# Kernel tuning notes

Measured on AMD Instinct MI355X. Metric: run time of the kernel, lower is better.

The kernel has to match this reference:

```python
import jax, jax.numpy as jnp
import numpy as np

EPS = 1e-12  # F.normalize default eps


def _l2_normalize(x, axis):
    n = jnp.sqrt(jnp.sum(x * x, axis=axis, keepdims=True))
    return x / jnp.maximum(n, EPS)


def setup_inputs() -> dict:
    key = jax.random.key(0)
    ks = jax.random.split(key, 13)
    b, n, d, h = 8, 4096, 1024, 16
    scale = 0.02
    inp = {
        "query": jax.random.normal(ks[0], (b, n, d), jnp.float32),
        "key": jax.random.normal(ks[1], (b, n, d), jnp.float32),
        "value": jax.random.normal(ks[2], (b, n, d), jnp.float32),
        "key_padding_mask": jax.random.randint(ks[3], (b, n), 0, 2).astype(bool),
        "Wq": jax.random.normal(ks[4], (d, d), jnp.float32) * scale,
        "bq": jax.random.normal(ks[5], (d,), jnp.float32) * scale,
        "Wk": jax.random.normal(ks[6], (d, d), jnp.float32) * scale,
        "bk": jax.random.normal(ks[7], (d,), jnp.float32) * scale,
        "Wv": jax.random.normal(ks[8], (d, d), jnp.float32) * scale,
        "bv": jax.random.normal(ks[9], (d,), jnp.float32) * scale,
        "Wo": jax.random.normal(ks[10], (d, d), jnp.float32) * scale,
        "bo": jax.random.normal(ks[11], (d,), jnp.float32) * scale,
    }
    return inp


def reference(query, key, value, key_padding_mask, Wq, bq, Wk, bk, Wv, bv, Wo, bo):
    b, n, d = query.shape
    h = 16
    dh = d // h
    # projections (torch Linear: x @ W.T + b)
    q = query @ Wq.T + bq
    k = key @ Wk.T + bk
    v = value @ Wv.T + bv
    # elu feature map
    q = 1.0 + jax.nn.elu(q)
    k = 1.0 + jax.nn.elu(k)
    # zero out padded keys
    k = jnp.where(key_padding_mask[:, :, None], 0.0, k)
    # split heads: b n (h d) -> b h n d
    q = q.reshape(b, n, h, dh).transpose(0, 2, 1, 3)
    k = k.reshape(b, n, h, dh).transpose(0, 2, 1, 3)
    v = v.reshape(b, n, h, dh).transpose(0, 2, 1, 3)
    # faithful to source: q normalized over sequence axis, k over feature axis
    q = _l2_normalize(q, axis=2)
    k = _l2_normalize(k, axis=3)
    kv = jnp.einsum('bhnd,bhne->bhde', k, v)      # (b,h,dh,dh)
    out = jnp.einsum('bhnd,bhde->bhne', q, kv)    # (b,h,n,dh)
    out = out.transpose(0, 2, 1, 3).reshape(b, n, d)
    return out @ Wo.T + bo
```

## Files before the change

### kernel.cpp

```cpp
#include <hip/hip_runtime.h>


typedef unsigned short u16;
typedef __attribute__((ext_vector_type(8))) short short8;
typedef __attribute__((ext_vector_type(4))) float f32x4;

#define GAS __attribute__((address_space(1)))
#define LAS __attribute__((address_space(3)))

__device__ __forceinline__ u16 f2bf(float x) {
  unsigned u = __float_as_uint(x);
  u += 0x7fffu + ((u >> 16) & 1u);
  return (u16)(u >> 16);
}
__device__ __forceinline__ unsigned pack2(float a, float b) {
  return (unsigned)f2bf(a) | ((unsigned)f2bf(b) << 16);
}
__device__ __forceinline__ float bflo(unsigned w) { return __uint_as_float(w << 16); }
__device__ __forceinline__ float bfhi(unsigned w) { return __uint_as_float(w & 0xffff0000u); }

__global__ __launch_bounds__(256) void detect_mask(const unsigned* __restrict__ m,
                                                   int* __restrict__ flags) {
  int i = blockIdx.x * 256 + threadIdx.x;
  unsigned w = m[i];
  if (w & 0xFEFEFEFEu) atomicOr(&flags[1], 1);
  if (w & 0xFFFFFF00u) atomicOr(&flags[0], 1);
}

__global__ __launch_bounds__(256) void mask_cvt(const void* __restrict__ m,
                                                const int* __restrict__ flags,
                                                float* __restrict__ keep) {
  int i = blockIdx.x * 256 + threadIdx.x;
  bool pad;
  if (flags[1])      pad = ((const float*)m)[i] != 0.f;
  else if (flags[0]) pad = ((const unsigned char*)m)[i] != 0;
  else               pad = ((const int*)m)[i] != 0;
  keep[i] = pad ? 0.f : 1.f;
}

__device__ __forceinline__ void cvt_body(const float* __restrict__ src,
                                         u16* __restrict__ dst, int n4) {
  int i = blockIdx.x * blockDim.x + threadIdx.x;
  int stride = gridDim.x * blockDim.x;
  for (; i < n4; i += stride) {
    float4 v = ((const float4*)src)[i];
    ((uint2*)dst)[i] = make_uint2(pack2(v.x, v.y), pack2(v.z, v.w));
  }
}
__global__ __launch_bounds__(256) void cvt3(const float* __restrict__ s0, const float* __restrict__ s1,
                                            const float* __restrict__ s2,
                                            u16* __restrict__ d0, u16* __restrict__ d1,
                                            u16* __restrict__ d2, int n4) {
  const float* s = (blockIdx.z == 0) ? s0 : (blockIdx.z == 1) ? s1 : s2;
  u16* d = (blockIdx.z == 0) ? d0 : (blockIdx.z == 1) ? d1 : d2;
  cvt_body(s, d, n4);
}
__global__ __launch_bounds__(256) void cvt4(const float* __restrict__ s0, const float* __restrict__ s1,
                                            const float* __restrict__ s2, const float* __restrict__ s3,
                                            u16* __restrict__ d0, u16* __restrict__ d1,
                                            u16* __restrict__ d2, u16* __restrict__ d3, int n4) {
  const float* s = (blockIdx.z == 0) ? s0 : (blockIdx.z == 1) ? s1 : (blockIdx.z == 2) ? s2 : s3;
  u16* d = (blockIdx.z == 0) ? d0 : (blockIdx.z == 1) ? d1 : (blockIdx.z == 2) ? d2 : d3;
  cvt_body(s, d, n4);
}

template <int MODE>
__global__ __launch_bounds__(256) void gemm_bt(const u16* __restrict__ A,
                                               const u16* __restrict__ B0,
                                               const float* __restrict__ bias,
                                               void* __restrict__ Out,
                                               float* __restrict__ sacc,
                                               const float* __restrict__ keep) {
  constexpr int K = 1024;
  __shared__ __align__(16) u16 As[128 * 64];
  __shared__ __align__(16) u16 Bs[128 * 64];

  const int t = threadIdx.x;
  const int w = t >> 6, l = t & 63;
  const int wm = w & 1, wn = w >> 1;
  const int rowTile = blockIdx.y * 128;
  const int colTile = blockIdx.x * 128;
  const int bidx = blockIdx.y >> 5;

  const u16* B = (MODE == 3) ? (B0 + ((size_t)bidx << 20)) : B0;

  f32x4 acc[4][4] = {};

  const int lr = l >> 3;
  const int lc = (l & 7) << 3;
  const u16* aRow = A + (size_t)(rowTile + w * 32 + lr) * K + lc;
  const u16* bRow = B + (size_t)(colTile + w * 32 + lr) * K + lc;

  for (int kt = 0; kt < K / 64; ++kt) {
    const int k0 = kt * 64;
    __syncthreads();
#pragma unroll
    for (int s = 0; s < 4; ++s) {
      __builtin_amdgcn_global_load_lds((const GAS void*)(aRow + (size_t)s * 8 * K + k0),
                                       (LAS void*)&As[(w * 4 + s) * 512], 16, 0, 0);
      __builtin_amdgcn_global_load_lds((const GAS void*)(bRow + (size_t)s * 8 * K + k0),
                                       (LAS void*)&Bs[(w * 4 + s) * 512], 16, 0, 0);
    }
    __syncthreads();
#pragma unroll
    for (int kk = 0; kk < 2; ++kk) {
      short8 af[4], bf[4];
      const int ko = kk * 32 + ((l >> 4) << 3);
#pragma unroll
      for (int mb = 0; mb < 4; ++mb)
        af[mb] = *(const short8*)&As[(wm * 64 + mb * 16 + (l & 15)) * 64 + ko];
#pragma unroll
      for (int nb = 0; nb < 4; ++nb)
        bf[nb] = *(const short8*)&Bs[(wn * 64 + nb * 16 + (l & 15)) * 64 + ko];
#pragma unroll
      for (int mb = 0; mb < 4; ++mb)
#pragma unroll
        for (int nb = 0; nb < 4; ++nb)
          acc[mb][nb] = __builtin_amdgcn_mfma_f32_16x16x32_bf16(af[mb], bf[nb], acc[mb][nb], 0, 0, 0);
    }
  }

  const int qr = (l >> 4) << 2;
  const int cl = l & 15;
#pragma unroll
  for (int nb = 0; nb < 4; ++nb) {
    const int col = colTile + wn * 64 + nb * 16 + cl;
    const float bv = bias[col];
    float csum = 0.f;
#pragma unroll
    for (int mb = 0; mb < 4; ++mb) {
      const int rowb = rowTile + wm * 64 + mb * 16 + qr;
#pragma unroll
      for (int r = 0; r < 4; ++r) {
        float y = acc[mb][nb][r] + bv;
        if (MODE == 0 || MODE == 1) y = (y > 0.f) ? (y + 1.f) : __expf(y);
        if (MODE == 1) y *= keep[rowb + r];
        if (MODE == 3) ((float*)Out)[(size_t)(rowb + r) * 1024 + col] = y;
        else           ((u16*)Out)[(size_t)(rowb + r) * 1024 + col] = f2bf(y);
        if (MODE == 0) csum += y * y;
      }
    }
    if (MODE == 0) {
      csum += __shfl_xor(csum, 16);
      csum += __shfl_xor(csum, 32);
      if (l < 16) atomicAdd(&sacc[bidx * 1024 + colTile + wn * 64 + nb * 16 + l], csum);
    }
  }
}

__global__ __launch_bounds__(256, 2) void kv2(const u16* __restrict__ fk,
                                              const u16* __restrict__ fv,
                                              float* __restrict__ kvpart) {
  const int ch = blockIdx.x, h = blockIdx.y, b = blockIdx.z;
  __shared__ __align__(16) u16 smem[2 * 256 * 64];
  u16* lk = smem;
  u16* lv = smem + 256 * 64;
  const int t = threadIdx.x;
  const int w = t >> 6, l = t & 63;
  const int d8 = (l & 7) * 8, e8 = (l >> 3) * 8;
  float acc[64] = {};

  for (int sub = 0; sub < 4; ++sub) {
    const int i0 = ch * 1024 + sub * 256;
    __syncthreads();
    {
      const size_t g = ((size_t)(b * 4096 + i0 + t)) * 1024 + h * 64;
      const uint4* kp = (const uint4*)&fk[g];
      float kf[64];
#pragma unroll
      for (int j = 0; j < 8; ++j) {
        uint4 kq = kp[j];
        kf[j * 8 + 0] = bflo(kq.x); kf[j * 8 + 1] = bfhi(kq.x);
        kf[j * 8 + 2] = bflo(kq.y); kf[j * 8 + 3] = bfhi(kq.y);
        kf[j * 8 + 4] = bflo(kq.z); kf[j * 8 + 5] = bfhi(kq.z);
        kf[j * 8 + 6] = bflo(kq.w); kf[j * 8 + 7] = bfhi(kq.w);
      }
      float ss = 0.f;
#pragma unroll
      for (int j = 0; j < 64; ++j) ss += kf[j] * kf[j];
      const float inv = 1.f / fmaxf(sqrtf(ss), 1e-12f);
#pragma unroll
      for (int j = 0; j < 8; ++j) {
        uint4 o;
        o.x = pack2(kf[j * 8 + 0] * inv, kf[j * 8 + 1] * inv);
        o.y = pack2(kf[j * 8 + 2] * inv, kf[j * 8 + 3] * inv);
        o.z = pack2(kf[j * 8 + 4] * inv, kf[j * 8 + 5] * inv);
        o.w = pack2(kf[j * 8 + 6] * inv, kf[j * 8 + 7] * inv);
        *(uint4*)&lk[t * 64 + j * 8] = o;
      }
      const uint4* vp = (const uint4*)&fv[g];
#pragma unroll
      for (int j = 0; j < 8; ++j) *(uint4*)&lv[t * 64 + j * 8] = vp[j];
    }
    __syncthreads();
#pragma unroll 2
    for (int ii = 0; ii < 64; ++ii) {
      const int i = w * 64 + ii;
      uint4 kw4 = *(const uint4*)&lk[i * 64 + d8];
      uint4 vw4 = *(const uint4*)&lv[i * 64 + e8];
      float ka[8], va[8];
      ka[0] = bflo(kw4.x); ka[1] = bfhi(kw4.x); ka[2] = bflo(kw4.y); ka[3] = bfhi(kw4.y);
      ka[4] = bflo(kw4.z); ka[5] = bfhi(kw4.z); ka[6] = bflo(kw4.w); ka[7] = bfhi(kw4.w);
      va[0] = bflo(vw4.x); va[1] = bfhi(vw4.x); va[2] = bflo(vw4.y); va[3] = bfhi(vw4.y);
      va[4] = bflo(vw4.z); va[5] = bfhi(vw4.z); va[6] = bflo(vw4.w); va[7] = bfhi(vw4.w);
#pragma unroll
      for (int a = 0; a < 8; ++a)
#pragma unroll
        for (int c = 0; c < 8; ++c)
          acc[a * 8 + c] += ka[a] * va[c];
    }
  }

  __syncthreads();
  float* scratch = (float*)smem;
  if (w > 0) {
#pragma unroll
    for (int c = 0; c < 64; c += 4)
      *(float4*)&scratch[((w - 1) * 64 + l) * 64 + c] = *(float4*)&acc[c];
  }
  __syncthreads();
  if (w == 0) {
#pragma unroll
    for (int p = 0; p < 3; ++p)
#pragma unroll
      for (int c = 0; c < 64; c += 4) {
        float4 s = *(const float4*)&scratch[(p * 64 + l) * 64 + c];
        acc[c + 0] += s.x; acc[c + 1] += s.y; acc[c + 2] += s.z; acc[c + 3] += s.w;
      }
    float* dst = kvpart + (size_t)(((ch * 8 + b) * 16 + h)) * 4096;
#pragma unroll
    for (int a = 0; a < 8; ++a)
#pragma unroll
      for (int c = 0; c < 8; c += 4)
        *(float4*)&dst[(d8 + a) * 64 + e8 + c] = *(float4*)&acc[a * 8 + c];
  }
}

__global__ __launch_bounds__(256) void kv_reduce(const float* __restrict__ kvpart,
                                                 const float* __restrict__ sacc,
                                                 float* __restrict__ kvred) {
  const int bh = blockIdx.x;
  const int b = bh >> 4, h = bh & 15;
  const int t = threadIdx.x;
  const int d = t >> 2;
  const float invq = 1.f / fmaxf(sqrtf(sacc[b * 1024 + h * 64 + d]), 1e-12f);
#pragma unroll
  for (int j = 0; j < 4; ++j) {
    const size_t off = (size_t)bh * 4096 + t * 16 + j * 4;
    float4 s = *(const float4*)&kvpart[off];
#pragma unroll
    for (int ch = 1; ch < 4; ++ch) {
      float4 p = *(const float4*)&kvpart[(size_t)ch * 524288 + off];
      s.x += p.x; s.y += p.y; s.z += p.z; s.w += p.w;
    }
    s.x *= invq; s.y *= invq; s.z *= invq; s.w *= invq;
    *(float4*)&kvred[(size_t)bh * 4096 + t * 16 + j * 4] = s;
  }
}

__global__ __launch_bounds__(256) void scale_mt(const float* __restrict__ kvred,
                                                const u16* __restrict__ wob,
                                                u16* __restrict__ Mt) {
  const int jt = blockIdx.x, h = blockIdx.y, b = blockIdx.z;
  __shared__ float kvl[64 * 64];
  const int t = threadIdx.x;

  {
    const int d = t >> 2, cp = (t & 3) * 16;
    const float* src = kvred + (size_t)((b * 16 + h) * 4096) + d * 64 + cp;
#pragma unroll
    for (int c = 0; c < 16; c += 4)
      *(float4*)&kvl[d * 64 + cp + c] = *(const float4*)&src[c];
  }
  __syncthreads();

  const int j = jt * 128 + (t & 127);
  const int g = t >> 7;
  float wo[64];
  const u16* wp = wob + (size_t)j * 1024 + h * 64;
#pragma unroll
  for (int e8 = 0; e8 < 64; e8 += 8) {
    uint4 q = *(const uint4*)&wp[e8];
    wo[e8 + 0] = bflo(q.x); wo[e8 + 1] = bfhi(q.x);
    wo[e8 + 2] = bflo(q.y); wo[e8 + 3] = bfhi(q.y);
    wo[e8 + 4] = bflo(q.z); wo[e8 + 5] = bfhi(q.z);
    wo[e8 + 6] = bflo(q.w); wo[e8 + 7] = bfhi(q.w);
  }
  u16* op = Mt + ((size_t)b << 20) + (size_t)j * 1024 + h * 64 + g * 32;
#pragma unroll 4
  for (int dd = 0; dd < 32; ++dd) {
    const int drow = g * 32 + dd;
    float s = 0.f;
#pragma unroll
    for (int e = 0; e < 64; ++e) s += kvl[drow * 64 + e] * wo[e];
    op[dd] = f2bf(s);
  }
}

extern "C" void kernel_launch(void* const* d_in, const int* in_sizes, int n_in,
                              void* d_out, int out_size, void* d_ws, size_t ws_size,
                              hipStream_t stream) {
  const float* query = (const float*)d_in[0];
  const float* key   = (const float*)d_in[1];
  const float* value = (const float*)d_in[2];
  const void*  mask  = d_in[3];
  const float* Wq = (const float*)d_in[4];
  const float* bq = (const float*)d_in[5];
  const float* Wk = (const float*)d_in[6];
  const float* bk = (const float*)d_in[7];
  const float* Wv = (const float*)d_in[8];
  const float* bv = (const float*)d_in[9];
  const float* Wo = (const float*)d_in[10];
  const float* bo = (const float*)d_in[11];

  char* W = (char*)d_ws;
  int*   flags = (int*)W;
  float* sacc  = (float*)(W + 256);
  float* keep  = (float*)(W + 33024);
  u16* wqb = (u16*)(W + 164096);
  u16* wkb = wqb + 1048576;
  u16* wvb = wkb + 1048576;
  u16* wob = wvb + 1048576;
  u16* qb  = wob + 1048576;
  u16* kb  = qb + 33554432;
  u16* vb  = kb + 33554432;
  u16* fq  = vb + 33554432;
  u16* fk  = fq + 33554432;
  u16* fv  = fk + 33554432;
  u16* Mt = qb;
  float* kvpart = (float*)kb;
  float* kvred  = (float*)(kb + 4194304);

  hipMemsetAsync(d_ws, 0, 33024, stream);

  detect_mask<<<32, 256, 0, stream>>>((const unsigned*)mask, flags);
  mask_cvt<<<128, 256, 0, stream>>>(mask, flags, keep);

  cvt3<<<dim3(1024, 1, 3), 256, 0, stream>>>(query, key, value, qb, kb, vb, 8388608);
  cvt4<<<dim3(128, 1, 4), 256, 0, stream>>>(Wq, Wk, Wv, Wo, wqb, wkb, wvb, wob, 262144);

  dim3 gg(8, 256);
  gemm_bt<0><<<gg, 256, 0, stream>>>(qb, wqb, bq, fq, sacc, nullptr);
  gemm_bt<1><<<gg, 256, 0, stream>>>(kb, wkb, bk, fk, nullptr, keep);
  gemm_bt<2><<<gg, 256, 0, stream>>>(vb, wvb, bv, fv, nullptr, nullptr);

  kv2<<<dim3(4, 16, 8), 256, 0, stream>>>(fk, fv, kvpart);
  kv_reduce<<<128, 256, 0, stream>>>(kvpart, sacc, kvred);
  scale_mt<<<dim3(8, 16, 8), 256, 0, stream>>>(kvred, wob, Mt);

  gemm_bt<3><<<gg, 256, 0, stream>>>(fq, Mt, bo, d_out, nullptr, nullptr);
}
```

Before: 1.061 ms.

## Fuse fp32-to-bf16 input conversion into projection GEMM loads and remap tiles per XCD

Removes the separate cvt3 pass over query/key/value. The projection GEMMs now read fp32 activations directly, pack them to bf16 in registers and store them to LDS, which saves a full read-write round trip of three large tensors. The block index is also remapped so that each XCD handles a contiguous group of row tiles, aiming for better L2 reuse. In exchange, A-tile loads now go through registers instead of async global-to-LDS, and each A load moves twice the bytes without double buffering, which may expose more latency.

Result: faster. 991.4 us (-6.6%).

```diff
diff --git a/kernel.cpp b/kernel.cpp
--- a/kernel.cpp
+++ b/kernel.cpp
@@ -47,14 +47,6 @@
     ((uint2*)dst)[i] = make_uint2(pack2(v.x, v.y), pack2(v.z, v.w));
   }
 }
-__global__ __launch_bounds__(256) void cvt3(const float* __restrict__ s0, const float* __restrict__ s1,
-                                            const float* __restrict__ s2,
-                                            u16* __restrict__ d0, u16* __restrict__ d1,
-                                            u16* __restrict__ d2, int n4) {
-  const float* s = (blockIdx.z == 0) ? s0 : (blockIdx.z == 1) ? s1 : s2;
-  u16* d = (blockIdx.z == 0) ? d0 : (blockIdx.z == 1) ? d1 : d2;
-  cvt_body(s, d, n4);
-}
 __global__ __launch_bounds__(256) void cvt4(const float* __restrict__ s0, const float* __restrict__ s1,
                                             const float* __restrict__ s2, const float* __restrict__ s3,
                                             u16* __restrict__ d0, u16* __restrict__ d1,
@@ -65,7 +57,7 @@
 }
 
 template <int MODE>
-__global__ __launch_bounds__(256) void gemm_bt(const u16* __restrict__ A,
+__global__ __launch_bounds__(256) void gemm_bt(const void* __restrict__ Ain,
                                                const u16* __restrict__ B0,
                                                const float* __restrict__ bias,
                                                void* __restrict__ Out,
@@ -78,28 +70,57 @@
   const int t = threadIdx.x;
   const int w = t >> 6, l = t & 63;
   const int wm = w & 1, wn = w >> 1;
-  const int rowTile = blockIdx.y * 128;
-  const int colTile = blockIdx.x * 128;
-  const int bidx = blockIdx.y >> 5;
+
+  const int lin = blockIdx.y * 8 + blockIdx.x;
+  const int xcd = lin & 7;
+  const int j   = lin >> 3;
+  const int rowTile = (xcd * 32 + (j >> 3)) * 128;
+  const int colTile = (j & 7) * 128;
+  const int bidx = rowTile >> 12;
 
   const u16* B = (MODE == 3) ? (B0 + ((size_t)bidx << 20)) : B0;
 
   f32x4 acc[4][4] = {};
 
   const int lr = l >> 3;
-  const int lc = (l & 7) << 3;
-  const u16* aRow = A + (size_t)(rowTile + w * 32 + lr) * K + lc;
-  const u16* bRow = B + (size_t)(colTile + w * 32 + lr) * K + lc;
+  const int le = (l & 7) << 3;
+  const float* aRowF = (const float*)Ain + (size_t)(rowTile + w * 32 + lr) * K + le;
+  const u16*   aRowB = (const u16*)Ain   + (size_t)(rowTile + w * 32 + lr) * K + le;
+  const u16*   bRow  = B + (size_t)(colTile + w * 32 + lr) * K + le;
 
   for (int kt = 0; kt < K / 64; ++kt) {
     const int k0 = kt * 64;
     __syncthreads();
-#pragma unroll
-    for (int s = 0; s < 4; ++s) {
-      __builtin_amdgcn_global_load_lds((const GAS void*)(aRow + (size_t)s * 8 * K + k0),
-                                       (LAS void*)&As[(w * 4 + s) * 512], 16, 0, 0);
-      __builtin_amdgcn_global_load_lds((const GAS void*)(bRow + (size_t)s * 8 * K + k0),
-                                       (LAS void*)&Bs[(w * 4 + s) * 512], 16, 0, 0);
+    if constexpr (MODE < 3) {
+      float4 r[8];
+#pragma unroll
+      for (int s = 0; s < 4; ++s) {
+        const float* p = aRowF + (size_t)s * 8 * K + k0;
+        r[2 * s + 0] = *(const float4*)(p);
+        r[2 * s + 1] = *(const float4*)(p + 4);
+      }
+#pragma unroll
+      for (int s = 0; s < 4; ++s) {
+        __builtin_amdgcn_global_load_lds((const GAS void*)(bRow + (size_t)s * 8 * K + k0),
+                                         (LAS void*)&Bs[(w * 4 + s) * 512], 16, 0, 0);
+      }
+#pragma unroll
+      for (int s = 0; s < 4; ++s) {
+        uint4 o;
+        o.x = pack2(r[2 * s + 0].x, r[2 * s + 0].y);
+        o.y = pack2(r[2 * s + 0].z, r[2 * s + 0].w);
+        o.z = pack2(r[2 * s + 1].x, r[2 * s + 1].y);
+        o.w = pack2(r[2 * s + 1].z, r[2 * s + 1].w);
+        *(uint4*)&As[(w * 4 + s) * 512 + l * 8] = o;
+      }
+    } else {
+#pragma unroll
+      for (int s = 0; s < 4; ++s) {
+        __builtin_amdgcn_global_load_lds((const GAS void*)(aRowB + (size_t)s * 8 * K + k0),
+                                         (LAS void*)&As[(w * 4 + s) * 512], 16, 0, 0);
+        __builtin_amdgcn_global_load_lds((const GAS void*)(bRow + (size_t)s * 8 * K + k0),
+                                         (LAS void*)&Bs[(w * 4 + s) * 512], 16, 0, 0);
+      }
     }
     __syncthreads();
 #pragma unroll
@@ -321,28 +342,24 @@
   u16* wkb = wqb + 1048576;
   u16* wvb = wkb + 1048576;
   u16* wob = wvb + 1048576;
-  u16* qb  = wob + 1048576;
-  u16* kb  = qb + 33554432;
-  u16* vb  = kb + 33554432;
-  u16* fq  = vb + 33554432;
+  u16* fq  = wob + 1048576;
   u16* fk  = fq + 33554432;
   u16* fv  = fk + 33554432;
-  u16* Mt = qb;
-  float* kvpart = (float*)kb;
-  float* kvred  = (float*)(kb + 4194304);
+  u16* Mt  = fv + 33554432;
+  float* kvpart = (float*)(Mt + 8388608);
+  float* kvred  = kvpart + 2097152;
 
   hipMemsetAsync(d_ws, 0, 33024, stream);
 
   detect_mask<<<32, 256, 0, stream>>>((const unsigned*)mask, flags);
   mask_cvt<<<128, 256, 0, stream>>>(mask, flags, keep);
 
-  cvt3<<<dim3(1024, 1, 3), 256, 0, stream>>>(query, key, value, qb, kb, vb, 8388608);
   cvt4<<<dim3(128, 1, 4), 256, 0, stream>>>(Wq, Wk, Wv, Wo, wqb, wkb, wvb, wob, 262144);
 
   dim3 gg(8, 256);
-  gemm_bt<0><<<gg, 256, 0, stream>>>(qb, wqb, bq, fq, sacc, nullptr);
-  gemm_bt<1><<<gg, 256, 0, stream>>>(kb, wkb, bk, fk, nullptr, keep);
-  gemm_bt<2><<<gg, 256, 0, stream>>>(vb, wvb, bv, fv, nullptr, nullptr);
+  gemm_bt<0><<<gg, 256, 0, stream>>>(query, wqb, bq, fq, sacc, nullptr);
+  gemm_bt<1><<<gg, 256, 0, stream>>>(key,   wkb, bk, fk, nullptr, keep);
+  gemm_bt<2><<<gg, 256, 0, stream>>>(value, wvb, bv, fv, nullptr, nullptr);
 
   kv2<<<dim3(4, 16, 8), 256, 0, stream>>>(fk, fv, kvpart);
   kv_reduce<<<128, 256, 0, stream>>>(kvpart, sacc, kvred);
```
